# Performance work log

Hardware: AMD Instinct MI355X
Metric: run time of the kernel (lower is better)

## Reference

```python
import jax, jax.numpy as jnp
import numpy as np

B, S, E, NH = 2, 2048, 1024, 8
DH = E // NH


def setup_inputs() -> dict:
    key = jax.random.key(0)
    ks = jax.random.split(key, 8)
    q = jax.random.normal(ks[0], (B, S, E), dtype=jnp.float32)
    k = jax.random.normal(ks[1], (B, S, E), dtype=jnp.float32)
    v = jax.random.normal(ks[2], (B, S, E), dtype=jnp.float32)
    # gate projections: Linear(3E -> NH)
    igate_w = jax.random.normal(ks[3], (NH, 3 * E), dtype=jnp.float32) * 0.02
    igate_b = jax.random.normal(ks[4], (NH,), dtype=jnp.float32) * 0.1
    fgate_w = jax.random.normal(ks[5], (NH, 3 * E), dtype=jnp.float32) * 0.02
    fgate_b = jnp.linspace(3.0, 6.0, NH, dtype=jnp.float32)  # bias_linspace_init_
    norm_weight = 1.0 + 0.01 * jax.random.normal(ks[6], (E,), dtype=jnp.float32)
    return {"q": q, "k": k, "v": v, "igate_w": igate_w, "igate_b": igate_b,
            "fgate_w": fgate_w, "fgate_b": fgate_b, "norm_weight": norm_weight}


def _mlstm_forward(q, k, v, igate_w, igate_b, fgate_w, fgate_b, norm_weight):
    eps = 1e-6
    gate_in = jnp.concatenate([q, k, v], axis=-1)            # (B,S,3E)
    i_pre = gate_in @ igate_w.T + igate_b                    # (B,S,NH)
    f_pre = gate_in @ fgate_w.T + fgate_b                    # (B,S,NH)
    i_pre = jnp.transpose(i_pre, (0, 2, 1))                  # (B,NH,S)
    f_pre = jnp.transpose(f_pre, (0, 2, 1))                  # (B,NH,S)

    qh = jnp.transpose(q.reshape(B, S, NH, DH), (0, 2, 1, 3))  # (B,NH,S,DH)
    kh = jnp.transpose(k.reshape(B, S, NH, DH), (0, 2, 1, 3))
    vh = jnp.transpose(v.reshape(B, S, NH, DH), (0, 2, 1, 3))

    # cumulative log forget gates; decay matrix D[i,j] = sum_{u=j+1..i} logsig(f_u) + i_pre[j]
    log_fg = jax.nn.log_sigmoid(f_pre)                       # (B,NH,S)
    cs = jnp.cumsum(log_fg, axis=-1)                         # (B,NH,S)
    diff = cs[:, :, :, None] - cs[:, :, None, :]             # (B,NH,S,S) = cs[i]-cs[j]
    causal = jnp.tril(jnp.ones((S, S), dtype=bool))
    log_fg_mat = jnp.where(causal, diff, -jnp.inf)
    log_D = log_fg_mat + i_pre[:, :, None, :]                # (B,NH,S,S)

    max_log_D = jnp.max(log_D, axis=-1, keepdims=True)       # rowwise stabilizer
    D = jnp.exp(log_D - max_log_D)

    qk = jnp.einsum("bhsd,bhtd->bhst", qh, kh / jnp.sqrt(jnp.float32(DH)))
    C = qk * D
    normalizer = jnp.maximum(jnp.abs(jnp.sum(C, axis=-1, keepdims=True)),
                             jnp.exp(-max_log_D))
    Cn = C / (normalizer + eps)
    h = jnp.einsum("bhst,bhtd->bhsd", Cn, vh)                # (B,NH,S,DH)

    # MultiHeadLayerNorm == group_norm(num_groups=NH): per-head, per-token over DH
    mu = jnp.mean(h, axis=-1, keepdims=True)
    var = jnp.var(h, axis=-1, keepdims=True)
    hn = (h - mu) / jnp.sqrt(var + 1e-5)
    hn = hn * norm_weight.reshape(NH, DH)[None, :, None, :]
    return jnp.transpose(hn, (0, 2, 1, 3)).reshape(B, S, E)


def reference(q, k, v, igate_w, igate_b, fgate_w, fgate_b, norm_weight):
    return _mlstm_forward(q, k, v, igate_w, igate_b, fgate_w, fgate_b, norm_weight)
```

## Files before the change

kernel.cpp:

```cpp
#include <hip/hip_runtime.h>
#include <hip/hip_bf16.h>
#include <math.h>

typedef __attribute__((ext_vector_type(8))) short bf16x8;
typedef __attribute__((ext_vector_type(16))) float f32x16;

namespace {
constexpr int kB = 2, kS = 2048, kE = 1024, kNH = 8, kDH = 128, kE3 = 3072;
constexpr float kLog2e = 1.4426950408889634f;
constexpr int kUnits = 27;
constexpr int kSplitPerBh = 20;
}

__device__ const int kOrder[kUnits] = {6,19,20,17,18,5,15,16,13,14,24,25,4,
                                       11,12,21,22,23,26,9,10,3,7,8,2,1,0};

__device__ __forceinline__ ushort f2bf(float x) {
  union { __hip_bfloat16 b; ushort u; } c; c.b = __float2bfloat16(x); return c.u;
}
__device__ __forceinline__ uint pk2(float a, float b) {
  return (uint)f2bf(a) | ((uint)f2bf(b) << 16);
}
__device__ __forceinline__ void gload16(const void* g, void* l) {
  __builtin_amdgcn_global_load_lds(
      (const __attribute__((address_space(1))) void*)g,
      (__attribute__((address_space(3))) void*)l, 16, 0, 0);
}
__device__ __forceinline__ f32x16 zero16() {
  f32x16 z;
#pragma unroll
  for (int i = 0; i < 16; ++i) z[i] = 0.f;
  return z;
}
union UB8 { uint4 u; bf16x8 f; };

__device__ __forceinline__ float butterfly64(float* acc, int lane) {
  int cur = 64;
#pragma unroll
  for (int lv = 0; lv < 6; ++lv) {
    const int bmask = 1 << lv;
    const int half = cur >> 1;
    const bool hi = (lane & bmask) != 0;
#pragma unroll
    for (int i = 0; i < 32; ++i) {
      if (i >= half) break;
      const float keep = hi ? acc[i + half] : acc[i];
      const float send = hi ? acc[i] : acc[i + half];
      acc[i] = keep + __shfl_xor(send, bmask);
    }
    cur = half;
  }
  return acc[0];
}

__global__ __launch_bounds__(256) void convkv_kernel(
    const float* __restrict__ k, const float* __restrict__ v,
    ushort* __restrict__ Kb, ushort* __restrict__ Vtb) {
  const int bh = blockIdx.y;
  const int b = bh >> 3, h = bh & 7;
  const int s0 = blockIdx.x * 32;
  const int tid = threadIdx.x;
  __shared__ ushort Vst[32 * 128];

  const int tl = tid >> 3;
  const int d0 = (tid & 7) * 16;
  const int s = s0 + tl;
  {
    const size_t base = ((size_t)b * kS + s) * kE + h * kDH + d0;
    const float4 k0 = *reinterpret_cast<const float4*>(k + base);
    const float4 k1 = *reinterpret_cast<const float4*>(k + base + 4);
    const float4 k2 = *reinterpret_cast<const float4*>(k + base + 8);
    const float4 k3 = *reinterpret_cast<const float4*>(k + base + 12);
    uint4 pa, pb;
    pa.x = pk2(k0.x, k0.y); pa.y = pk2(k0.z, k0.w);
    pa.z = pk2(k1.x, k1.y); pa.w = pk2(k1.z, k1.w);
    pb.x = pk2(k2.x, k2.y); pb.y = pk2(k2.z, k2.w);
    pb.z = pk2(k3.x, k3.y); pb.w = pk2(k3.z, k3.w);
    ushort* kd = Kb + ((size_t)bh * kS + s) * 128 + d0;
    *reinterpret_cast<uint4*>(kd) = pa;
    *reinterpret_cast<uint4*>(kd + 8) = pb;

    const float4 v0 = *reinterpret_cast<const float4*>(v + base);
    const float4 v1 = *reinterpret_cast<const float4*>(v + base + 4);
    const float4 v2 = *reinterpret_cast<const float4*>(v + base + 8);
    const float4 v3 = *reinterpret_cast<const float4*>(v + base + 12);
    uint4 va, vb4;
    va.x = pk2(v0.x, v0.y); va.y = pk2(v0.z, v0.w);
    va.z = pk2(v1.x, v1.y); va.w = pk2(v1.z, v1.w);
    vb4.x = pk2(v2.x, v2.y); vb4.y = pk2(v2.z, v2.w);
    vb4.z = pk2(v3.x, v3.y); vb4.w = pk2(v3.z, v3.w);
    const int c0 = d0 >> 3;
    char* row = reinterpret_cast<char*>(Vst) + tl * 256;
    *reinterpret_cast<uint4*>(row + (((c0 + 0) ^ (tl & 15)) << 4)) = va;
    *reinterpret_cast<uint4*>(row + (((c0 + 1) ^ (tl & 15)) << 4)) = vb4;
  }
  __syncthreads();

  {
    const int d = tid >> 1, half = tid & 1;
    const int cd = d >> 3;
    const int od = (d & 7) * 2;
    uint tmp[8];
#pragma unroll
    for (int p = 0; p < 8; ++p) {
      const int t = half * 16 + 2 * p;
      const ushort u0 = *reinterpret_cast<const ushort*>(
          reinterpret_cast<const char*>(Vst) + t * 256 + ((cd ^ (t & 15)) << 4) + od);
      const ushort u1 = *reinterpret_cast<const ushort*>(
          reinterpret_cast<const char*>(Vst) + (t + 1) * 256 + ((cd ^ ((t + 1) & 15)) << 4) + od);
      tmp[p] = (uint)u0 | ((uint)u1 << 16);
    }
    ushort* vd = Vtb + ((size_t)bh * kDH + d) * kS + s0 + half * 16;
    uint4 o0, o1;
    o0.x = tmp[0]; o0.y = tmp[1]; o0.z = tmp[2]; o0.w = tmp[3];
    o1.x = tmp[4]; o1.y = tmp[5]; o1.z = tmp[6]; o1.w = tmp[7];
    *reinterpret_cast<uint4*>(vd) = o0;
    *reinterpret_cast<uint4*>(vd + 8) = o1;
  }
}

__global__ __launch_bounds__(256) void gates_kernel(
    const float* __restrict__ q, const float* __restrict__ k, const float* __restrict__ v,
    const float* __restrict__ iw, const float* __restrict__ ib,
    const float* __restrict__ fw, const float* __restrict__ fb,
    float* __restrict__ i_pre, float* __restrict__ f_pre) {
  const int tid = threadIdx.x;
  const int w = tid >> 6, lane = tid & 63;
  const int tokbase = blockIdx.x * 4;
  float acc[64];
#pragma unroll
  for (int i = 0; i < 64; ++i) acc[i] = 0.f;

  for (int step = 0; step < 12; ++step) {
    const int e = w * 768 + step * 64 + lane;
    const int seg = e >> 10;
    const int eo = e & 1023;
    const float* __restrict__ src = (seg == 0) ? q : (seg == 1) ? k : v;
    float gv[4];
#pragma unroll
    for (int t = 0; t < 4; ++t)
      gv[t] = src[(size_t)(tokbase + t) * kE + eo];
    float wi[8], wf[8];
#pragma unroll
    for (int hh = 0; hh < 8; ++hh) {
      wi[hh] = iw[hh * kE3 + e];
      wf[hh] = fw[hh * kE3 + e];
    }
#pragma unroll
    for (int t = 0; t < 4; ++t) {
#pragma unroll
      for (int hh = 0; hh < 8; ++hh) {
        acc[t * 16 + hh]     += gv[t] * wi[hh];
        acc[t * 16 + 8 + hh] += gv[t] * wf[hh];
      }
    }
  }
  const float r = butterfly64(acc, lane);
  const int a = ((lane & 1) << 5) | ((lane & 2) << 3) | ((lane & 4) << 1) |
                ((lane & 8) >> 1) | ((lane & 16) >> 3) | ((lane & 32) >> 5);
  __shared__ float red[4][64];
  red[w][a] = r;
  __syncthreads();
  if (tid < 64) {
    const float val = red[0][tid] + red[1][tid] + red[2][tid] + red[3][tid];
    const int t = tid >> 4, gate = tid & 15, hh = gate & 7;
    const int token = tokbase + t;
    const int b = token >> 11, s = token & 2047;
    const size_t idx = ((size_t)(b * 8 + hh)) * kS + s;
    if (gate < 8) i_pre[idx] = val + ib[hh];
    else          f_pre[idx] = val + fb[hh];
  }
}

__global__ __launch_bounds__(256) void scan_kernel(
    const float* __restrict__ i_pre, const float* __restrict__ f_pre,
    float* __restrict__ wt_out, float* __restrict__ M2_out, float* __restrict__ nfl_out,
    float* __restrict__ Cg) {
  const int bh = blockIdx.x;
  const int tid = threadIdx.x;
  const int w = tid >> 6, lane = tid & 63;
  __shared__ float wsum[4], wmax[4];
  const float* __restrict__ fp = f_pre + (size_t)bh * kS;
  const float* __restrict__ ip = i_pre + (size_t)bh * kS;
  const int s0 = tid * 8;

  const float4 fa = *reinterpret_cast<const float4*>(fp + s0);
  const float4 fb4 = *reinterpret_cast<const float4*>(fp + s0 + 4);
  float lf[8];
  {
    const float fv[8] = {fa.x, fa.y, fa.z, fa.w, fb4.x, fb4.y, fb4.z, fb4.w};
#pragma unroll
    for (int j = 0; j < 8; ++j)
      lf[j] = fminf(fv[j], 0.f) - log1pf(expf(-fabsf(fv[j])));
  }
  float run = 0.f, pcs[8];
#pragma unroll
  for (int j = 0; j < 8; ++j) { run += lf[j]; pcs[j] = run; }
  float x = run;
#pragma unroll
  for (int d = 1; d < 64; d <<= 1) {
    const float t = __shfl_up(x, d);
    if (lane >= d) x += t;
  }
  if (lane == 63) wsum[w] = x;
  __syncthreads();
  float woff = 0.f;
#pragma unroll
  for (int i = 0; i < 4; ++i) if (i < w) woff += wsum[i];
  const float csbase = woff + x - run;
  float cs[8];
#pragma unroll
  for (int j = 0; j < 8; ++j) cs[j] = csbase + pcs[j];

  const float4 ia = *reinterpret_cast<const float4*>(ip + s0);
  const float4 ib4 = *reinterpret_cast<const float4*>(ip + s0 + 4);
  float av[8];
  {
    const float iv[8] = {ia.x, ia.y, ia.z, ia.w, ib4.x, ib4.y, ib4.z, ib4.w};
#pragma unroll
    for (int j = 0; j < 8; ++j) av[j] = iv[j] - cs[j];
  }
  float rmax = -1e30f, pm[8];
#pragma unroll
  for (int j = 0; j < 8; ++j) { rmax = fmaxf(rmax, av[j]); pm[j] = rmax; }

  float tm = rmax;
  tm = fmaxf(tm, __shfl_xor(tm, 1));
  tm = fmaxf(tm, __shfl_xor(tm, 2));
  tm = fmaxf(tm, __shfl_xor(tm, 4));
  if ((lane & 7) == 0) Cg[bh * 32 + (tid >> 3)] = tm * kLog2e;

  float4 wtlo, wthi;
  wtlo.x = exp2f((av[0] - tm) * kLog2e); wtlo.y = exp2f((av[1] - tm) * kLog2e);
  wtlo.z = exp2f((av[2] - tm) * kLog2e); wtlo.w = exp2f((av[3] - tm) * kLog2e);
  wthi.x = exp2f((av[4] - tm) * kLog2e); wthi.y = exp2f((av[5] - tm) * kLog2e);
  wthi.z = exp2f((av[6] - tm) * kLog2e); wthi.w = exp2f((av[7] - tm) * kLog2e);

  float mi = rmax;
#pragma unroll
  for (int d = 1; d < 64; d <<= 1) {
    const float t = __shfl_up(mi, d);
    if (lane >= d) mi = fmaxf(mi, t);
  }
  if (lane == 63) wmax[w] = mi;
  float mexcl = __shfl_up(mi, 1);
  if (lane == 0) mexcl = -1e30f;
  __syncthreads();
  float wmoff = -1e30f;
#pragma unroll
  for (int i = 0; i < 4; ++i) if (i < w) wmoff = fmaxf(wmoff, wmax[i]);
  const float mbase = fmaxf(wmoff, mexcl);

  float M[8];
#pragma unroll
  for (int j = 0; j < 8; ++j) M[j] = fmaxf(mbase, pm[j]);
  float4 m2lo, m2hi, nflo, nfhi;
  m2lo.x = M[0] * kLog2e; m2lo.y = M[1] * kLog2e; m2lo.z = M[2] * kLog2e; m2lo.w = M[3] * kLog2e;
  m2hi.x = M[4] * kLog2e; m2hi.y = M[5] * kLog2e; m2hi.z = M[6] * kLog2e; m2hi.w = M[7] * kLog2e;
  nflo.x = expf(-(cs[0] + M[0])); nflo.y = expf(-(cs[1] + M[1]));
  nflo.z = expf(-(cs[2] + M[2])); nflo.w = expf(-(cs[3] + M[3]));
  nfhi.x = expf(-(cs[4] + M[4])); nfhi.y = expf(-(cs[5] + M[5]));
  nfhi.z = expf(-(cs[6] + M[6])); nfhi.w = expf(-(cs[7] + M[7]));
  const size_t o = (size_t)bh * kS + s0;
  *reinterpret_cast<float4*>(wt_out + o) = wtlo;
  *reinterpret_cast<float4*>(wt_out + o + 4) = wthi;
  *reinterpret_cast<float4*>(M2_out + o) = m2lo;
  *reinterpret_cast<float4*>(M2_out + o + 4) = m2hi;
  *reinterpret_cast<float4*>(nfl_out + o) = nflo;
  *reinterpret_cast<float4*>(nfl_out + o + 4) = nfhi;
}

__global__ __launch_bounds__(256, 2) void attn_mfma_kernel(
    const float* __restrict__ qg, const ushort* __restrict__ Kb,
    const ushort* __restrict__ Vtb, const float* __restrict__ wt,
    const float* __restrict__ Cg, const float* __restrict__ M2,
    const float* __restrict__ nfl, const float* __restrict__ nw,
    float* __restrict__ out, float* __restrict__ ph, float* __restrict__ prs) {
  const int id = blockIdx.x;
  const int r8 = id & 7, qq = id >> 3;
  const int bh = r8 + 8 * (qq & 1);
  const int u = kOrder[qq >> 1];
  const int b = bh >> 3, h = bh & 7;
  int it, j0, j1, cid = -1;
  if (u <= 6) { it = u; const int T = 2 * it + 2; j0 = 0; j1 = T - 1; }
  else if (u <= 20) {
    const int s = u - 7; it = 7 + (s >> 1); const int ci = s & 1;
    const int T = 2 * it + 2;
    j0 = (T * ci) >> 1; j1 = ((T * (ci + 1)) >> 1) - 1;
    cid = bh * kSplitPerBh + (u - 7);
  } else {
    const int s = u - 21; it = 14 + (s >= 3 ? 1 : 0); const int ci = s - (s >= 3 ? 3 : 0);
    const int T = 2 * it + 2;
    j0 = (T * ci) / 3; j1 = (T * (ci + 1)) / 3 - 1;
    cid = bh * kSplitPerBh + (u - 7);
  }
  const int tid = threadIdx.x;
  const int w = tid >> 6, lane = tid & 63;
  const int l31 = lane & 31, hi = lane >> 5;
  const int row_w = it * 128 + w * 32;
  const int ig = row_w + l31;
  const size_t bhS = (size_t)bh * kS;

  __shared__ ushort Klds[2 * 64 * 128];
  __shared__ ushort Vlds[2 * 128 * 64];

  const char* __restrict__ KgBase = reinterpret_cast<const char*>(Kb + bhS * 128);
  const char* __restrict__ VgBase = reinterpret_cast<const char*>(Vtb + (size_t)bh * 128 * kS);
  const float* __restrict__ wtb = wt + bhS;

  bf16x8 qf[8];
  {
    const float scale = 0.08838834764831845f;
    const float* qrow = qg + ((size_t)b * kS + ig) * kE + h * kDH;
#pragma unroll
    for (int ks = 0; ks < 8; ++ks) {
      const int d0 = ks * 16 + hi * 8;
      const float4 lo = *reinterpret_cast<const float4*>(qrow + d0);
      const float4 hi4 = *reinterpret_cast<const float4*>(qrow + d0 + 4);
      UB8 f;
      f.u.x = pk2(lo.x * scale, lo.y * scale);
      f.u.y = pk2(lo.z * scale, lo.w * scale);
      f.u.z = pk2(hi4.x * scale, hi4.y * scale);
      f.u.w = pk2(hi4.z * scale, hi4.w * scale);
      qf[ks] = f.f;
    }
  }
  const float M2i = M2[bhS + ig];
  const float cgreg = Cg[bh * 32 + l31];

  int koffG[4], voffG[4];
#pragma unroll
  for (int i = 0; i < 4; ++i) {
    const int L = tid * 16 + i * 4096;
    { const int j = L >> 8, c = (L >> 4) & 15;
      koffG[i] = j * 256 + ((c ^ (j & 15)) << 4); }
    { const int d = L >> 7, c = (L >> 4) & 7;
      voffG[i] = d * 4096 + ((c ^ (d & 7)) << 4); }
  }
  auto stage = [&](int buf, int jt) {
    const char* Kg = KgBase + (size_t)jt * 16384;
    const char* Vg = VgBase + (size_t)jt * 128;
    char* kl = reinterpret_cast<char*>(Klds) + buf * 16384 + tid * 16;
    char* vl = reinterpret_cast<char*>(Vlds) + buf * 16384 + tid * 16;
#pragma unroll
    for (int i = 0; i < 4; ++i) gload16(Kg + koffG[i], kl + i * 4096);
#pragma unroll
    for (int i = 0; i < 4; ++i) gload16(Vg + voffG[i], vl + i * 4096);
  };

  f32x16 hacc[4];
#pragma unroll
  for (int dc = 0; dc < 4; ++dc) hacc[dc] = zero16();
  float rs = 0.f;

  float wtc0 = wtb[j0 * 64 + l31];
  float wtc1 = wtb[j0 * 64 + 32 + l31];
  stage(0, j0);
  __syncthreads();

  for (int jt = j0; jt <= j1; ++jt) {
    const int cur = (jt - j0) & 1;
    float wtn0, wtn1;
    if (jt < j1) {
      stage(cur ^ 1, jt + 1);
      wtn0 = wtb[(jt + 1) * 64 + l31];
      wtn1 = wtb[(jt + 1) * 64 + 32 + l31];
    }
    const int jlo = jt * 64;
    const bool v0 = (jlo <= row_w + 31);
    const bool v1 = (jlo + 32 <= row_w + 31);
    const bool fullmask = (jlo + 63 <= row_w);

    if (v0) {
      const float f = exp2f(__shfl(cgreg, jt) - M2i);
      const char* kb = reinterpret_cast<const char*>(Klds) + cur * 16384;
      const char* vb = reinterpret_cast<const char*>(Vlds) + cur * 16384;
      const int ksw = (l31 & 15) << 4;

      f32x16 sacc0 = zero16(), sacc1 = zero16();
#pragma unroll
      for (int ks = 0; ks < 8; ++ks) {
        const int colb = 32 * ks + 16 * hi;
        const bf16x8 kf0 = *reinterpret_cast<const bf16x8*>(
            kb + l31 * 256 + (colb ^ ksw));
        sacc0 = __builtin_amdgcn_mfma_f32_32x32x16_bf16(kf0, qf[ks], sacc0, 0, 0, 0);
        if (v1) {
          const bf16x8 kf1 = *reinterpret_cast<const bf16x8*>(
              kb + (32 + l31) * 256 + (colb ^ ksw));
          sacc1 = __builtin_amdgcn_mfma_f32_32x32x16_bf16(kf1, qf[ks], sacc1, 0, 0, 0);
        }
      }

      uint pkw[2][8];
#pragma unroll
      for (int jc = 0; jc < 2; ++jc) {
        if (jc == 1 && !v1) break;
        const f32x16 sa = jc ? sacc1 : sacc0;
        float p[16];
#pragma unroll
        for (int r = 0; r < 16; ++r) {
          const int c = (r & 3) + 8 * (r >> 2);
          const float wv = __shfl(jc ? wtc1 : wtc0, c + 4 * hi);
          float val = sa[r] * (wv * f);
          if (!fullmask) val = (jlo + jc * 32 + c + 4 * hi <= ig) ? val : 0.f;
          rs += val; p[r] = val;
        }
#pragma unroll
        for (int q2 = 0; q2 < 8; ++q2) pkw[jc][q2] = pk2(p[2 * q2], p[2 * q2 + 1]);
      }

#pragma unroll
      for (int ks = 0; ks < 4; ++ks) {
        const int jc = ks >> 1, ks2 = ks & 1;
        if (jc == 1 && !v1) break;
        UB8 pf;
        pf.u.x = pkw[jc][ks2 * 4 + 0]; pf.u.y = pkw[jc][ks2 * 4 + 1];
        pf.u.z = pkw[jc][ks2 * 4 + 2]; pf.u.w = pkw[jc][ks2 * 4 + 3];
        const int colb = 64 * jc + 32 * ks2 + 8 * hi;
#pragma unroll
        for (int dc = 0; dc < 4; ++dc) {
          const int d = dc * 32 + l31;
          const char* vrow = vb + d * 128;
          const int sw = (d & 7) << 4;
          const uint2 a = *reinterpret_cast<const uint2*>(vrow + (colb ^ sw));
          const uint2 c = *reinterpret_cast<const uint2*>(vrow + ((colb + 16) ^ sw));
          UB8 vf; vf.u.x = a.x; vf.u.y = a.y; vf.u.z = c.x; vf.u.w = c.y;
          hacc[dc] = __builtin_amdgcn_mfma_f32_32x32x16_bf16(pf.f, vf.f, hacc[dc], 0, 0, 0);
        }
      }
    }
    __syncthreads();
    if (jt < j1) { wtc0 = wtn0; wtc1 = wtn1; }
  }

  const float rs_tot = rs + __shfl_xor(rs, 32);

  if (cid >= 0) {
    float* pb = ph + (size_t)cid * 16384;
#pragma unroll
    for (int dc = 0; dc < 4; ++dc)
#pragma unroll
      for (int r = 0; r < 16; ++r) {
        const int il = w * 32 + (r & 3) + 8 * (r >> 2) + 4 * hi;
        pb[il * 128 + dc * 32 + l31] = hacc[dc][r];
      }
    if (hi == 0) prs[cid * 128 + w * 32 + l31] = rs_tot;
    return;
  }

  float nwv[4];
#pragma unroll
  for (int dc = 0; dc < 4; ++dc) nwv[dc] = nw[h * kDH + dc * 32 + l31];
#pragma unroll
  for (int r = 0; r < 16; ++r) {
    const int imap = (r & 3) + 8 * (r >> 2) + 4 * hi;
    const float rsum = __shfl(rs_tot, imap);
    const float nf = nfl[bhS + row_w + imap];
    const float inv = 1.f / (fmaxf(fabsf(rsum), nf) + 1e-6f);
    float hv[4];
    float s1 = 0.f, s2 = 0.f;
#pragma unroll
    for (int dc = 0; dc < 4; ++dc) {
      hv[dc] = hacc[dc][r] * inv;
      s1 += hv[dc]; s2 += hv[dc] * hv[dc];
    }
#pragma unroll
    for (int off = 1; off <= 16; off <<= 1) {
      s1 += __shfl_xor(s1, off);
      s2 += __shfl_xor(s2, off);
    }
    const float mu = s1 * (1.f / 128.f);
    const float var = s2 * (1.f / 128.f) - mu * mu;
    const float rstd = rsqrtf(var + 1e-5f);
    float* __restrict__ orow = out + ((size_t)b * kS + row_w + imap) * kE + h * kDH;
#pragma unroll
    for (int dc = 0; dc < 4; ++dc)
      orow[dc * 32 + l31] = (hv[dc] - mu) * rstd * nwv[dc];
  }
}

__global__ __launch_bounds__(256) void combine_kernel(
    const float* __restrict__ ph, const float* __restrict__ prs,
    const float* __restrict__ nfl, const float* __restrict__ nw,
    float* __restrict__ out) {
  const int blk = blockIdx.x;
  const int bh = blk / 9, ct = blk % 9;
  const int b = bh >> 3, h = bh & 7;
  const int it = 7 + ct;
  const int nc = (ct < 7) ? 2 : 3;
  const int cb0 = bh * kSplitPerBh + ((ct < 7) ? ct * 2 : 14 + (ct - 7) * 3);
  const int tid = threadIdx.x;
  __shared__ float sinv[128];
  if (tid < 128) {
    float rsum = 0.f;
    for (int c = 0; c < nc; ++c) rsum += prs[(cb0 + c) * 128 + tid];
    const float nf = nfl[(size_t)bh * kS + it * 128 + tid];
    sinv[tid] = 1.f / (fmaxf(fabsf(rsum), nf) + 1e-6f);
  }
  __syncthreads();
  for (int kk = 0; kk < 16; ++kk) {
    const int idx = kk * 256 + tid;
    const int row = idx >> 5, c4 = idx & 31;
    float ax = 0.f, ay = 0.f, az = 0.f, aw = 0.f;
    for (int c = 0; c < nc; ++c) {
      const float4 t = *reinterpret_cast<const float4*>(
          ph + (size_t)(cb0 + c) * 16384 + row * 128 + c4 * 4);
      ax += t.x; ay += t.y; az += t.z; aw += t.w;
    }
    const float inv = sinv[row];
    ax *= inv; ay *= inv; az *= inv; aw *= inv;
    float s1 = ax + ay + az + aw;
    float s2 = ax * ax + ay * ay + az * az + aw * aw;
#pragma unroll
    for (int off = 1; off <= 16; off <<= 1) {
      s1 += __shfl_xor(s1, off);
      s2 += __shfl_xor(s2, off);
    }
    const float mu = s1 * (1.f / 128.f);
    const float var = s2 * (1.f / 128.f) - mu * mu;
    const float rstd = rsqrtf(var + 1e-5f);
    const float4 nw4 = *reinterpret_cast<const float4*>(nw + h * kDH + c4 * 4);
    float4 o;
    o.x = (ax - mu) * rstd * nw4.x;
    o.y = (ay - mu) * rstd * nw4.y;
    o.z = (az - mu) * rstd * nw4.z;
    o.w = (aw - mu) * rstd * nw4.w;
    *reinterpret_cast<float4*>(
        out + ((size_t)b * kS + it * 128 + row) * kE + h * kDH + c4 * 4) = o;
  }
}

extern "C" void kernel_launch(void* const* d_in, const int* in_sizes, int n_in,
                              void* d_out, int out_size, void* d_ws, size_t ws_size,
                              hipStream_t stream) {
  const float* q  = (const float*)d_in[0];
  const float* k  = (const float*)d_in[1];
  const float* v  = (const float*)d_in[2];
  const float* iw = (const float*)d_in[3];
  const float* ib = (const float*)d_in[4];
  const float* fw = (const float*)d_in[5];
  const float* fb = (const float*)d_in[6];
  const float* nw = (const float*)d_in[7];
  float* out = (float*)d_out;

  char* ws = (char*)d_ws;
  const int BHS = kB * kNH * kS;
  float* i_pre = (float*)ws;
  float* f_pre = i_pre + BHS;
  float* wt    = i_pre + 2 * BHS;
  float* M2    = i_pre + 3 * BHS;
  float* nfl   = i_pre + 4 * BHS;
  float* Cg    = i_pre + 5 * BHS;
  ushort* Kb  = (ushort*)(ws + (size_t)(5 * BHS + 512) * 4);
  ushort* Vtb = Kb + (size_t)kB * kNH * kS * kDH;
  float* ph   = (float*)(Vtb + (size_t)kB * kNH * kS * kDH);
  float* prs  = ph + (size_t)320 * 128 * 128;

  convkv_kernel<<<dim3(kS / 32, kB * kNH), dim3(256), 0, stream>>>(k, v, Kb, Vtb);
  gates_kernel<<<dim3(kB * kS / 4), dim3(256), 0, stream>>>(q, k, v, iw, ib, fw, fb,
                                                            i_pre, f_pre);
  scan_kernel<<<dim3(kB * kNH), dim3(256), 0, stream>>>(i_pre, f_pre, wt, M2, nfl, Cg);
  attn_mfma_kernel<<<dim3(kUnits * kB * kNH), dim3(256), 0, stream>>>(
      q, Kb, Vtb, wt, Cg, M2, nfl, nw, out, ph, prs);
  combine_kernel<<<dim3(kB * kNH * 9), dim3(256), 0, stream>>>(ph, prs, nfl, nw, out);
}
```

Before: 123.0 us.

## Merge K/V conversion and gate kernels; single-buffer attention LDS with staged gate weights

The separate bf16 K/V conversion kernel and the gate projection kernel become one launch, with block ranges choosing the role, to save a launch and let both kinds of work run concurrently. The attention kernel drops LDS double buffering and syncs before and after each tile load, halving LDS use (possibly raising occupancy). It also stages the per-column decay weights into LDS with async loads and reads them as float4 instead of per-element shuffles. The cost is that global-to-LDS load latency is no longer overlapped with MFMA work inside a block.

```diff
diff --git a/kernel.cpp b/kernel.cpp
--- a/kernel.cpp
+++ b/kernel.cpp
@@ -53,122 +53,120 @@
   return acc[0];
 }
 
-__global__ __launch_bounds__(256) void convkv_kernel(
-    const float* __restrict__ k, const float* __restrict__ v,
-    ushort* __restrict__ Kb, ushort* __restrict__ Vtb) {
-  const int bh = blockIdx.y;
-  const int b = bh >> 3, h = bh & 7;
-  const int s0 = blockIdx.x * 32;
-  const int tid = threadIdx.x;
-  __shared__ ushort Vst[32 * 128];
-
-  const int tl = tid >> 3;
-  const int d0 = (tid & 7) * 16;
-  const int s = s0 + tl;
-  {
-    const size_t base = ((size_t)b * kS + s) * kE + h * kDH + d0;
-    const float4 k0 = *reinterpret_cast<const float4*>(k + base);
-    const float4 k1 = *reinterpret_cast<const float4*>(k + base + 4);
-    const float4 k2 = *reinterpret_cast<const float4*>(k + base + 8);
-    const float4 k3 = *reinterpret_cast<const float4*>(k + base + 12);
-    uint4 pa, pb;
-    pa.x = pk2(k0.x, k0.y); pa.y = pk2(k0.z, k0.w);
-    pa.z = pk2(k1.x, k1.y); pa.w = pk2(k1.z, k1.w);
-    pb.x = pk2(k2.x, k2.y); pb.y = pk2(k2.z, k2.w);
-    pb.z = pk2(k3.x, k3.y); pb.w = pk2(k3.z, k3.w);
-    ushort* kd = Kb + ((size_t)bh * kS + s) * 128 + d0;
-    *reinterpret_cast<uint4*>(kd) = pa;
-    *reinterpret_cast<uint4*>(kd + 8) = pb;
-
-    const float4 v0 = *reinterpret_cast<const float4*>(v + base);
-    const float4 v1 = *reinterpret_cast<const float4*>(v + base + 4);
-    const float4 v2 = *reinterpret_cast<const float4*>(v + base + 8);
-    const float4 v3 = *reinterpret_cast<const float4*>(v + base + 12);
-    uint4 va, vb4;
-    va.x = pk2(v0.x, v0.y); va.y = pk2(v0.z, v0.w);
-    va.z = pk2(v1.x, v1.y); va.w = pk2(v1.z, v1.w);
-    vb4.x = pk2(v2.x, v2.y); vb4.y = pk2(v2.z, v2.w);
-    vb4.z = pk2(v3.x, v3.y); vb4.w = pk2(v3.z, v3.w);
-    const int c0 = d0 >> 3;
-    char* row = reinterpret_cast<char*>(Vst) + tl * 256;
-    *reinterpret_cast<uint4*>(row + (((c0 + 0) ^ (tl & 15)) << 4)) = va;
-    *reinterpret_cast<uint4*>(row + (((c0 + 1) ^ (tl & 15)) << 4)) = vb4;
-  }
-  __syncthreads();
-
-  {
-    const int d = tid >> 1, half = tid & 1;
-    const int cd = d >> 3;
-    const int od = (d & 7) * 2;
-    uint tmp[8];
-#pragma unroll
-    for (int p = 0; p < 8; ++p) {
-      const int t = half * 16 + 2 * p;
-      const ushort u0 = *reinterpret_cast<const ushort*>(
-          reinterpret_cast<const char*>(Vst) + t * 256 + ((cd ^ (t & 15)) << 4) + od);
-      const ushort u1 = *reinterpret_cast<const ushort*>(
-          reinterpret_cast<const char*>(Vst) + (t + 1) * 256 + ((cd ^ ((t + 1) & 15)) << 4) + od);
-      tmp[p] = (uint)u0 | ((uint)u1 << 16);
-    }
-    ushort* vd = Vtb + ((size_t)bh * kDH + d) * kS + s0 + half * 16;
-    uint4 o0, o1;
-    o0.x = tmp[0]; o0.y = tmp[1]; o0.z = tmp[2]; o0.w = tmp[3];
-    o1.x = tmp[4]; o1.y = tmp[5]; o1.z = tmp[6]; o1.w = tmp[7];
-    *reinterpret_cast<uint4*>(vd) = o0;
-    *reinterpret_cast<uint4*>(vd + 8) = o1;
-  }
-}
-
-__global__ __launch_bounds__(256) void gates_kernel(
+__global__ __launch_bounds__(256) void prep_kernel(
     const float* __restrict__ q, const float* __restrict__ k, const float* __restrict__ v,
     const float* __restrict__ iw, const float* __restrict__ ib,
     const float* __restrict__ fw, const float* __restrict__ fb,
+    ushort* __restrict__ Kb, ushort* __restrict__ Vtb,
     float* __restrict__ i_pre, float* __restrict__ f_pre) {
+  const int bid = blockIdx.x;
   const int tid = threadIdx.x;
-  const int w = tid >> 6, lane = tid & 63;
-  const int tokbase = blockIdx.x * 4;
-  float acc[64];
-#pragma unroll
-  for (int i = 0; i < 64; ++i) acc[i] = 0.f;
-
-  for (int step = 0; step < 12; ++step) {
-    const int e = w * 768 + step * 64 + lane;
-    const int seg = e >> 10;
-    const int eo = e & 1023;
-    const float* __restrict__ src = (seg == 0) ? q : (seg == 1) ? k : v;
-    float gv[4];
-#pragma unroll
-    for (int t = 0; t < 4; ++t)
-      gv[t] = src[(size_t)(tokbase + t) * kE + eo];
-    float wi[8], wf[8];
-#pragma unroll
-    for (int hh = 0; hh < 8; ++hh) {
-      wi[hh] = iw[hh * kE3 + e];
-      wf[hh] = fw[hh * kE3 + e];
-    }
-#pragma unroll
-    for (int t = 0; t < 4; ++t) {
+  __shared__ ushort Vst[32 * 128];
+  __shared__ float red[4][64];
+
+  if (bid < 1024) {
+    const int bh = bid >> 6;
+    const int b = bh >> 3, h = bh & 7;
+    const int s0 = (bid & 63) * 32;
+    const int tl = tid >> 3;
+    const int d0 = (tid & 7) * 16;
+    const int s = s0 + tl;
+    {
+      const size_t base = ((size_t)b * kS + s) * kE + h * kDH + d0;
+      const float4 k0 = *reinterpret_cast<const float4*>(k + base);
+      const float4 k1 = *reinterpret_cast<const float4*>(k + base + 4);
+      const float4 k2 = *reinterpret_cast<const float4*>(k + base + 8);
+      const float4 k3 = *reinterpret_cast<const float4*>(k + base + 12);
+      uint4 pa, pb;
+      pa.x = pk2(k0.x, k0.y); pa.y = pk2(k0.z, k0.w);
+      pa.z = pk2(k1.x, k1.y); pa.w = pk2(k1.z, k1.w);
+      pb.x = pk2(k2.x, k2.y); pb.y = pk2(k2.z, k2.w);
+      pb.z = pk2(k3.x, k3.y); pb.w = pk2(k3.z, k3.w);
+      ushort* kd = Kb + ((size_t)bh * kS + s) * 128 + d0;
+      *reinterpret_cast<uint4*>(kd) = pa;
+      *reinterpret_cast<uint4*>(kd + 8) = pb;
+
+      const float4 v0 = *reinterpret_cast<const float4*>(v + base);
+      const float4 v1 = *reinterpret_cast<const float4*>(v + base + 4);
+      const float4 v2 = *reinterpret_cast<const float4*>(v + base + 8);
+      const float4 v3 = *reinterpret_cast<const float4*>(v + base + 12);
+      uint4 va, vb4;
+      va.x = pk2(v0.x, v0.y); va.y = pk2(v0.z, v0.w);
+      va.z = pk2(v1.x, v1.y); va.w = pk2(v1.z, v1.w);
+      vb4.x = pk2(v2.x, v2.y); vb4.y = pk2(v2.z, v2.w);
+      vb4.z = pk2(v3.x, v3.y); vb4.w = pk2(v3.z, v3.w);
+      const int c0 = d0 >> 3;
+      char* row = reinterpret_cast<char*>(Vst) + tl * 256;
+      *reinterpret_cast<uint4*>(row + (((c0 + 0) ^ (tl & 15)) << 4)) = va;
+      *reinterpret_cast<uint4*>(row + (((c0 + 1) ^ (tl & 15)) << 4)) = vb4;
+    }
+    __syncthreads();
+    {
+      const int d = tid >> 1, half = tid & 1;
+      const int cd = d >> 3;
+      const int od = (d & 7) * 2;
+      uint tmp[8];
+#pragma unroll
+      for (int p = 0; p < 8; ++p) {
+        const int t = half * 16 + 2 * p;
+        const ushort u0 = *reinterpret_cast<const ushort*>(
+            reinterpret_cast<const char*>(Vst) + t * 256 + ((cd ^ (t & 15)) << 4) + od);
+        const ushort u1 = *reinterpret_cast<const ushort*>(
+            reinterpret_cast<const char*>(Vst) + (t + 1) * 256 + ((cd ^ ((t + 1) & 15)) << 4) + od);
+        tmp[p] = (uint)u0 | ((uint)u1 << 16);
+      }
+      ushort* vd = Vtb + ((size_t)bh * kDH + d) * kS + s0 + half * 16;
+      uint4 o0, o1;
+      o0.x = tmp[0]; o0.y = tmp[1]; o0.z = tmp[2]; o0.w = tmp[3];
+      o1.x = tmp[4]; o1.y = tmp[5]; o1.z = tmp[6]; o1.w = tmp[7];
+      *reinterpret_cast<uint4*>(vd) = o0;
+      *reinterpret_cast<uint4*>(vd + 8) = o1;
+    }
+  } else {
+    const int w = tid >> 6, lane = tid & 63;
+    const int tokbase = (bid - 1024) * 4;
+    float acc[64];
+#pragma unroll
+    for (int i = 0; i < 64; ++i) acc[i] = 0.f;
+
+    for (int step = 0; step < 12; ++step) {
+      const int e = w * 768 + step * 64 + lane;
+      const int seg = e >> 10;
+      const int eo = e & 1023;
+      const float* __restrict__ src = (seg == 0) ? q : (seg == 1) ? k : v;
+      float gv[4];
+#pragma unroll
+      for (int t = 0; t < 4; ++t)
+        gv[t] = src[(size_t)(tokbase + t) * kE + eo];
+      float wi[8], wf[8];
 #pragma unroll
       for (int hh = 0; hh < 8; ++hh) {
-        acc[t * 16 + hh]     += gv[t] * wi[hh];
-        acc[t * 16 + 8 + hh] += gv[t] * wf[hh];
-      }
-    }
-  }
-  const float r = butterfly64(acc, lane);
-  const int a = ((lane & 1) << 5) | ((lane & 2) << 3) | ((lane & 4) << 1) |
-                ((lane & 8) >> 1) | ((lane & 16) >> 3) | ((lane & 32) >> 5);
-  __shared__ float red[4][64];
-  red[w][a] = r;
-  __syncthreads();
-  if (tid < 64) {
-    const float val = red[0][tid] + red[1][tid] + red[2][tid] + red[3][tid];
-    const int t = tid >> 4, gate = tid & 15, hh = gate & 7;
-    const int token = tokbase + t;
-    const int b = token >> 11, s = token & 2047;
-    const size_t idx = ((size_t)(b * 8 + hh)) * kS + s;
-    if (gate < 8) i_pre[idx] = val + ib[hh];
-    else          f_pre[idx] = val + fb[hh];
+        wi[hh] = iw[hh * kE3 + e];
+        wf[hh] = fw[hh * kE3 + e];
+      }
+#pragma unroll
+      for (int t = 0; t < 4; ++t) {
+#pragma unroll
+        for (int hh = 0; hh < 8; ++hh) {
+          acc[t * 16 + hh]     += gv[t] * wi[hh];
+          acc[t * 16 + 8 + hh] += gv[t] * wf[hh];
+        }
+      }
+    }
+    const float r = butterfly64(acc, lane);
+    const int a = ((lane & 1) << 5) | ((lane & 2) << 3) | ((lane & 4) << 1) |
+                  ((lane & 8) >> 1) | ((lane & 16) >> 3) | ((lane & 32) >> 5);
+    red[w][a] = r;
+    __syncthreads();
+    if (tid < 64) {
+      const float val = red[0][tid] + red[1][tid] + red[2][tid] + red[3][tid];
+      const int t = tid >> 4, gate = tid & 15, hh = gate & 7;
+      const int token = tokbase + t;
+      const int b = token >> 11, s = token & 2047;
+      const size_t idx = ((size_t)(b * 8 + hh)) * kS + s;
+      if (gate < 8) i_pre[idx] = val + ib[hh];
+      else          f_pre[idx] = val + fb[hh];
+    }
   }
 }
 
@@ -301,12 +299,13 @@
   const int ig = row_w + l31;
   const size_t bhS = (size_t)bh * kS;
 
-  __shared__ ushort Klds[2 * 64 * 128];
-  __shared__ ushort Vlds[2 * 128 * 64];
+  __shared__ ushort Klds[64 * 128];
+  __shared__ ushort Vlds[128 * 64];
+  __shared__ float Wtl[64];
 
   const char* __restrict__ KgBase = reinterpret_cast<const char*>(Kb + bhS * 128);
   const char* __restrict__ VgBase = reinterpret_cast<const char*>(Vtb + (size_t)bh * 128 * kS);
-  const float* __restrict__ wtb = wt + bhS;
+  const char* __restrict__ WgBase = reinterpret_cast<const char*>(wt + bhS);
 
   bf16x8 qf[8];
   {
@@ -337,15 +336,18 @@
     { const int d = L >> 7, c = (L >> 4) & 7;
       voffG[i] = d * 4096 + ((c ^ (d & 7)) << 4); }
   }
-  auto stage = [&](int buf, int jt) {
+  auto stage = [&](int jt) {
     const char* Kg = KgBase + (size_t)jt * 16384;
     const char* Vg = VgBase + (size_t)jt * 128;
-    char* kl = reinterpret_cast<char*>(Klds) + buf * 16384 + tid * 16;
-    char* vl = reinterpret_cast<char*>(Vlds) + buf * 16384 + tid * 16;
+    char* kl = reinterpret_cast<char*>(Klds) + tid * 16;
+    char* vl = reinterpret_cast<char*>(Vlds) + tid * 16;
 #pragma unroll
     for (int i = 0; i < 4; ++i) gload16(Kg + koffG[i], kl + i * 4096);
 #pragma unroll
     for (int i = 0; i < 4; ++i) gload16(Vg + voffG[i], vl + i * 4096);
+    if (tid < 16)
+      gload16(WgBase + jt * 256 + tid * 16,
+              reinterpret_cast<char*>(Wtl) + tid * 16);
   };
 
   f32x16 hacc[4];
@@ -353,84 +355,79 @@
   for (int dc = 0; dc < 4; ++dc) hacc[dc] = zero16();
   float rs = 0.f;
 
-  float wtc0 = wtb[j0 * 64 + l31];
-  float wtc1 = wtb[j0 * 64 + 32 + l31];
-  stage(0, j0);
-  __syncthreads();
-
   for (int jt = j0; jt <= j1; ++jt) {
-    const int cur = (jt - j0) & 1;
-    float wtn0, wtn1;
-    if (jt < j1) {
-      stage(cur ^ 1, jt + 1);
-      wtn0 = wtb[(jt + 1) * 64 + l31];
-      wtn1 = wtb[(jt + 1) * 64 + 32 + l31];
-    }
+    __syncthreads();
+    stage(jt);
+    __syncthreads();
+
     const int jlo = jt * 64;
     const bool v0 = (jlo <= row_w + 31);
     const bool v1 = (jlo + 32 <= row_w + 31);
     const bool fullmask = (jlo + 63 <= row_w);
-
-    if (v0) {
-      const float f = exp2f(__shfl(cgreg, jt) - M2i);
-      const char* kb = reinterpret_cast<const char*>(Klds) + cur * 16384;
-      const char* vb = reinterpret_cast<const char*>(Vlds) + cur * 16384;
-      const int ksw = (l31 & 15) << 4;
-
-      f32x16 sacc0 = zero16(), sacc1 = zero16();
-#pragma unroll
-      for (int ks = 0; ks < 8; ++ks) {
-        const int colb = 32 * ks + 16 * hi;
-        const bf16x8 kf0 = *reinterpret_cast<const bf16x8*>(
-            kb + l31 * 256 + (colb ^ ksw));
-        sacc0 = __builtin_amdgcn_mfma_f32_32x32x16_bf16(kf0, qf[ks], sacc0, 0, 0, 0);
-        if (v1) {
-          const bf16x8 kf1 = *reinterpret_cast<const bf16x8*>(
-              kb + (32 + l31) * 256 + (colb ^ ksw));
-          sacc1 = __builtin_amdgcn_mfma_f32_32x32x16_bf16(kf1, qf[ks], sacc1, 0, 0, 0);
-        }
-      }
-
-      uint pkw[2][8];
-#pragma unroll
-      for (int jc = 0; jc < 2; ++jc) {
-        if (jc == 1 && !v1) break;
-        const f32x16 sa = jc ? sacc1 : sacc0;
-        float p[16];
-#pragma unroll
-        for (int r = 0; r < 16; ++r) {
-          const int c = (r & 3) + 8 * (r >> 2);
-          const float wv = __shfl(jc ? wtc1 : wtc0, c + 4 * hi);
-          float val = sa[r] * (wv * f);
+    if (!v0) continue;
+
+    const float f = exp2f(__shfl(cgreg, jt) - M2i);
+    const char* kb = reinterpret_cast<const char*>(Klds);
+    const char* vb = reinterpret_cast<const char*>(Vlds);
+    const int ksw = (l31 & 15) << 4;
+
+    f32x16 sacc0 = zero16(), sacc1 = zero16();
+#pragma unroll
+    for (int ks = 0; ks < 8; ++ks) {
+      const int colb = 32 * ks + 16 * hi;
+      const bf16x8 kf0 = *reinterpret_cast<const bf16x8*>(
+          kb + l31 * 256 + (colb ^ ksw));
+      sacc0 = __builtin_amdgcn_mfma_f32_32x32x16_bf16(kf0, qf[ks], sacc0, 0, 0, 0);
+      if (v1) {
+        const bf16x8 kf1 = *reinterpret_cast<const bf16x8*>(
+            kb + (32 + l31) * 256 + (colb ^ ksw));
+        sacc1 = __builtin_amdgcn_mfma_f32_32x32x16_bf16(kf1, qf[ks], sacc1, 0, 0, 0);
+      }
+    }
+
+    uint pkw[2][8];
+#pragma unroll
+    for (int jc = 0; jc < 2; ++jc) {
+      if (jc == 1 && !v1) break;
+      const f32x16 sa = jc ? sacc1 : sacc0;
+      float p[16];
+#pragma unroll
+      for (int q2 = 0; q2 < 4; ++q2) {
+        const float4 wq = *reinterpret_cast<const float4*>(
+            &Wtl[jc * 32 + q2 * 8 + 4 * hi]);
+        const float wv[4] = {wq.x, wq.y, wq.z, wq.w};
+#pragma unroll
+        for (int m = 0; m < 4; ++m) {
+          const int r = q2 * 4 + m;
+          const int c = m + 8 * q2;
+          float val = sa[r] * (wv[m] * f);
           if (!fullmask) val = (jlo + jc * 32 + c + 4 * hi <= ig) ? val : 0.f;
           rs += val; p[r] = val;
         }
-#pragma unroll
-        for (int q2 = 0; q2 < 8; ++q2) pkw[jc][q2] = pk2(p[2 * q2], p[2 * q2 + 1]);
-      }
-
-#pragma unroll
-      for (int ks = 0; ks < 4; ++ks) {
-        const int jc = ks >> 1, ks2 = ks & 1;
-        if (jc == 1 && !v1) break;
-        UB8 pf;
-        pf.u.x = pkw[jc][ks2 * 4 + 0]; pf.u.y = pkw[jc][ks2 * 4 + 1];
-        pf.u.z = pkw[jc][ks2 * 4 + 2]; pf.u.w = pkw[jc][ks2 * 4 + 3];
-        const int colb = 64 * jc + 32 * ks2 + 8 * hi;
-#pragma unroll
-        for (int dc = 0; dc < 4; ++dc) {
-          const int d = dc * 32 + l31;
-          const char* vrow = vb + d * 128;
-          const int sw = (d & 7) << 4;
-          const uint2 a = *reinterpret_cast<const uint2*>(vrow + (colb ^ sw));
-          const uint2 c = *reinterpret_cast<const uint2*>(vrow + ((colb + 16) ^ sw));
-          UB8 vf; vf.u.x = a.x; vf.u.y = a.y; vf.u.z = c.x; vf.u.w = c.y;
-          hacc[dc] = __builtin_amdgcn_mfma_f32_32x32x16_bf16(pf.f, vf.f, hacc[dc], 0, 0, 0);
-        }
-      }
-    }
-    __syncthreads();
-    if (jt < j1) { wtc0 = wtn0; wtc1 = wtn1; }
+      }
+#pragma unroll
+      for (int q2 = 0; q2 < 8; ++q2) pkw[jc][q2] = pk2(p[2 * q2], p[2 * q2 + 1]);
+    }
+
+#pragma unroll
+    for (int ks = 0; ks < 4; ++ks) {
+      const int jc = ks >> 1, ks2 = ks & 1;
+      if (jc == 1 && !v1) break;
+      UB8 pf;
+      pf.u.x = pkw[jc][ks2 * 4 + 0]; pf.u.y = pkw[jc][ks2 * 4 + 1];
+      pf.u.z = pkw[jc][ks2 * 4 + 2]; pf.u.w = pkw[jc][ks2 * 4 + 3];
+      const int colb = 64 * jc + 32 * ks2 + 8 * hi;
+#pragma unroll
+      for (int dc = 0; dc < 4; ++dc) {
+        const int d = dc * 32 + l31;
+        const char* vrow = vb + d * 128;
+        const int sw = (d & 7) << 4;
+        const uint2 a = *reinterpret_cast<const uint2*>(vrow + (colb ^ sw));
+        const uint2 c = *reinterpret_cast<const uint2*>(vrow + ((colb + 16) ^ sw));
+        UB8 vf; vf.u.x = a.x; vf.u.y = a.y; vf.u.z = c.x; vf.u.w = c.y;
+        hacc[dc] = __builtin_amdgcn_mfma_f32_32x32x16_bf16(pf.f, vf.f, hacc[dc], 0, 0, 0);
+      }
+    }
   }
 
   const float rs_tot = rs + __shfl_xor(rs, 32);
@@ -556,9 +553,8 @@
   float* ph   = (float*)(Vtb + (size_t)kB * kNH * kS * kDH);
   float* prs  = ph + (size_t)320 * 128 * 128;
 
-  convkv_kernel<<<dim3(kS / 32, kB * kNH), dim3(256), 0, stream>>>(k, v, Kb, Vtb);
-  gates_kernel<<<dim3(kB * kS / 4), dim3(256), 0, stream>>>(q, k, v, iw, ib, fw, fb,
-                                                            i_pre, f_pre);
+  prep_kernel<<<dim3(2048), dim3(256), 0, stream>>>(q, k, v, iw, ib, fw, fb,
+                                                    Kb, Vtb, i_pre, f_pre);
   scan_kernel<<<dim3(kB * kNH), dim3(256), 0, stream>>>(i_pre, f_pre, wt, M2, nfl, Cg);
   attn_mfma_kernel<<<dim3(kUnits * kB * kNH), dim3(256), 0, stream>>>(
       q, Kb, Vtb, wt, Cg, M2, nfl, nw, out, ph, prs);
```

Result: faster. 115.2 us (-6.4%).
